# Kernel tuning notes

Hardware: AMD Instinct MI355X
Metric: run time of the kernel (lower is better)

The kernel has to match this reference:

```python
import jax, jax.numpy as jnp
import numpy as np

N_NODES = 20000
N_EDGES = 200000
MUL = 16          # multiplicity of 0e and 1o in irreps_in/out
NUM_BASIS = 8
HIDDEN = 64
W_NUMEL = 4 * MUL * MUL  # 1024: four 'uvw' paths of 16x1x16 weights
INV_SQRT3 = 1.0 / np.sqrt(3.0)
PW0 = np.sqrt(1.0 / 32.0)  # path weight into 0e: sqrt(dim(0e)/(16+16))
PW1 = np.sqrt(3.0 / 32.0)  # path weight into 1o: sqrt(dim(1o)/(16+16))
SI_NORM = 1.0 / np.sqrt(MUL)  # o3.Linear fan-in normalization


def setup_inputs() -> dict:
    key = jax.random.key(0)
    ks = jax.random.split(key, 12)
    node_feat = jax.random.normal(ks[0], (N_NODES, 4 * MUL), dtype=jnp.float32)
    edge_attr = jax.random.uniform(ks[1], (N_EDGES, NUM_BASIS), dtype=jnp.float32)
    sh = jax.random.normal(ks[2], (N_EDGES, 4), dtype=jnp.float32)
    edge_index = jax.random.randint(ks[3], (2, N_EDGES), 0, N_NODES, dtype=jnp.int32)
    # radial MLP params (torch nn.Linear: y = x @ W.T + b; we store W already transposed)
    w1 = jax.random.normal(ks[4], (NUM_BASIS, HIDDEN), dtype=jnp.float32) * 0.3
    b1 = jax.random.normal(ks[5], (HIDDEN,), dtype=jnp.float32) * 0.1
    w2 = jax.random.normal(ks[6], (HIDDEN, W_NUMEL), dtype=jnp.float32) * 0.1
    b2 = jax.random.normal(ks[7], (W_NUMEL,), dtype=jnp.float32) * 0.1
    # o3.Linear self-interaction: one (mul_in, mul_out) block per irrep
    wsi0 = jax.random.normal(ks[8], (MUL, MUL), dtype=jnp.float32)
    wsi1 = jax.random.normal(ks[9], (MUL, MUL), dtype=jnp.float32)
    return {"node_feat": node_feat, "edge_attr": edge_attr, "sh": sh,
            "w1": w1, "b1": b1, "w2": w2, "b2": b2,
            "wsi0": wsi0, "wsi1": wsi1, "edge_index": edge_index}


def reference(node_feat, edge_attr, sh, w1, b1, w2, b2, wsi0, wsi1, edge_index):
    n_nodes = node_feat.shape[0]
    row, col = edge_index[0], edge_index[1]

    # per-edge tensor-product weights from radial basis
    h = jax.nn.silu(edge_attr @ w1 + b1)
    w = h @ w2 + b2                                   # [E, 1024]
    Wp = w.reshape(-1, 4, MUL, MUL)                    # 4 paths, each (u, w)

    # gathered source-node features, split into 0e scalars and 1o vectors
    xs = node_feat[col, :MUL]                          # [E, 16]
    xv = node_feat[col, MUL:].reshape(-1, MUL, 3)      # [E, 16, 3]
    y0 = sh[:, 0]                                      # [E]   0e part of sh
    y1 = sh[:, 1:4]                                    # [E,3] 1o part of sh

    # CG paths (e3nn FullyConnectedTensorProduct, component/element norm):
    # path0: 0e x 0e -> 0e (cg=1); path3: 1o x 1o -> 0e (cg=delta/sqrt3)
    dot = jnp.einsum('eum,em->eu', xv, y1)             # [E,16]
    out0 = PW0 * (jnp.einsum('euw,eu->ew', Wp[:, 0], xs * y0[:, None])
                  + INV_SQRT3 * jnp.einsum('euw,eu->ew', Wp[:, 3], dot))
    # path1: 0e x 1o -> 1o; path2: 1o x 0e -> 1o (cg=delta/sqrt3)
    outv = (PW1 * INV_SQRT3) * (
        jnp.einsum('euw,eu->ew', Wp[:, 1], xs)[:, :, None] * y1[:, None, :]
        + jnp.einsum('euw,eum->ewm', Wp[:, 2], xv) * y0[:, None, None])

    messages = jnp.concatenate([out0, outv.reshape(-1, 3 * MUL)], axis=-1)  # [E,64]
    agg = jax.ops.segment_sum(messages, row, num_segments=n_nodes)          # [N,64]

    # self-interaction: o3.Linear (block-diagonal per irrep, / sqrt(fan_in))
    si0 = (node_feat[:, :MUL] @ wsi0) * SI_NORM
    siv = jnp.einsum('num,uw->nwm', node_feat[:, MUL:].reshape(-1, MUL, 3), wsi1) * SI_NORM
    si = jnp.concatenate([si0, siv.reshape(-1, 3 * MUL)], axis=-1)
    return agg + si
```

## Files before the change

### kernel.cpp

```cpp
#include <hip/hip_runtime.h>
#include <hip/hip_bf16.h>

#define N_NODES_C 20000
#define N_EDGES_C 200000

#define PW0_C       0.17677669529663687f
#define PW1_C       0.30618621784789724f
#define INV_SQRT3_C 0.57735026918962576f
#define SI_NORM_C   0.25f

typedef __attribute__((ext_vector_type(8))) short short8;
typedef __attribute__((ext_vector_type(4))) float f32x4;

__device__ __forceinline__ unsigned short f2bf(float x) {
    union { float f; unsigned u; } v; v.f = x;
    unsigned r = v.u + 0x7fffu + ((v.u >> 16) & 1u);
    return (unsigned short)(r >> 16);
}

__global__ __launch_bounds__(256) void k_h(const float* __restrict__ ea,
                                           const float* __restrict__ w1,
                                           const float* __restrict__ b1,
                                           unsigned short* __restrict__ h) {
    int idx = blockIdx.x * 256 + threadIdx.x;
    int e = idx >> 6, c = idx & 63;
    const float* a = ea + e * 8;
    float acc = b1[c];
    #pragma unroll
    for (int k = 0; k < 8; ++k) acc = fmaf(a[k], w1[k * 64 + c], acc);
    float s = acc / (1.0f + __expf(-acc));
    h[idx] = f2bf(s);
}

__global__ __launch_bounds__(256) void k_w2(const float* __restrict__ w2,
                                            unsigned short* __restrict__ w2f) {
    int tid = blockIdx.x * 256 + threadIdx.x;
    int j  = tid & 7;
    int l  = (tid >> 3) & 63;
    int ks = (tid >> 9) & 1;
    int tp = tid >> 10;
    int u = tp >> 2, k = tp & 3;
    int krow = ks * 32 + (l >> 4) * 8 + j;
    int col  = k * 256 + u * 16 + (l & 15);
    w2f[tid] = f2bf(w2[krow * 1024 + col]);
}

__global__ __launch_bounds__(256) void k_count(const int* __restrict__ ei,
                                               int* __restrict__ cnt) {
    int e = blockIdx.x * 256 + threadIdx.x;
    if (e < N_EDGES_C) atomicAdd(&cnt[ei[e]], 1);
}

__global__ __launch_bounds__(1024) void k_scan(const int* __restrict__ cnt,
                                               int* __restrict__ base) {
    __shared__ int wsum[16];
    __shared__ int carry_s;
    if (threadIdx.x == 0) carry_s = 0;
    int lane = threadIdx.x & 63, wid = threadIdx.x >> 6;
    __syncthreads();
    for (int start = 0; start < N_NODES_C; start += 1024) {
        int i = start + threadIdx.x;
        int v = (i < N_NODES_C) ? cnt[i] : 0;
        int x = v;
        #pragma unroll
        for (int d = 1; d < 64; d <<= 1) {
            int y = __shfl_up(x, d);
            if (lane >= d) x += y;
        }
        if (lane == 63) wsum[wid] = x;
        __syncthreads();
        int woff = 0;
        #pragma unroll
        for (int w = 0; w < 16; ++w) if (w < wid) woff += wsum[w];
        int carry = carry_s;
        if (i < N_NODES_C) base[i] = carry + woff + x - v;
        __syncthreads();
        if (threadIdx.x == 1023) carry_s = carry + woff + x;
    }
    if (threadIdx.x == 0) base[N_NODES_C] = N_EDGES_C;
}

__global__ __launch_bounds__(256) void k_fill(const int* __restrict__ ei,
                                              const int* __restrict__ base,
                                              int* __restrict__ cur,
                                              int* __restrict__ eix) {
    int e = blockIdx.x * 256 + threadIdx.x;
    if (e < N_EDGES_C) {
        int r = ei[e];
        int p = atomicAdd(&cur[r], 1);
        eix[base[r] + p] = e;
    }
}

__global__ __launch_bounds__(256, 2) void k_main(const float* __restrict__ nf,
                                                 const float* __restrict__ sh,
                                                 const int* __restrict__ ei,
                                                 const unsigned short* __restrict__ h,
                                                 const unsigned short* __restrict__ w2f,
                                                 const float* __restrict__ b2,
                                                 float* __restrict__ msg) {
    __shared__ __align__(16) char uni[24576];
    __shared__ float S[6][16][64];
    __shared__ float sh_s[64][4];
    __shared__ float b2_s[4][16][16];

    float (*nf_s)[64] = (float (*)[64])uni;
    float (*P0)[16]   = (float (*)[16])uni;
    float (*P1)[16]   = (float (*)[16])(uni + 4096);
    float (*P3)[16]   = (float (*)[16])(uni + 8192);
    float (*Q)[64][16] = (float (*)[64][16])(uni + 12288);

    const int t    = threadIdx.x;
    const int e0   = blockIdx.x * 64;
    const int lane = t & 63;
    const int wid  = t >> 6;

    {
        float* b2flat = &b2_s[0][0][0];
        #pragma unroll
        for (int i = 0; i < 4; ++i) b2flat[t + i * 256] = b2[t + i * 256];
        int el = t >> 2, part = t & 3;
        int col = ei[N_EDGES_C + e0 + el];
        const f32x4* src = (const f32x4*)(nf + col * 64);
        #pragma unroll
        for (int q = 0; q < 4; ++q)
            *(f32x4*)&nf_s[el][part * 16 + q * 4] = src[part * 4 + q];
        if (part == 0)
            *(f32x4*)&sh_s[el][0] = *(const f32x4*)(sh + (e0 + el) * 4);
    }
    short8 B0[16], B1[16];
    {
        const unsigned short* wk = w2f + wid * 1024 + lane * 8;
        #pragma unroll
        for (int u = 0; u < 16; ++u) {
            B0[u] = *(const short8*)&wk[u * 4096];
            B1[u] = *(const short8*)&wk[u * 4096 + 512];
        }
    }
    __syncthreads();

    {
        int el = t >> 2, part = t & 3;
        float y0 = sh_s[el][0], y1x = sh_s[el][1], y1y = sh_s[el][2], y1z = sh_s[el][3];
        #pragma unroll
        for (int uu = 0; uu < 4; ++uu) {
            int u = part * 4 + uu;
            float xs = nf_s[el][u];
            float v0 = nf_s[el][16 + u * 3 + 0];
            float v1 = nf_s[el][16 + u * 3 + 1];
            float v2 = nf_s[el][16 + u * 3 + 2];
            float dot = v0 * y1x + v1 * y1y + v2 * y1z;
            S[0][u][el] = xs * y0;
            S[1][u][el] = xs;
            S[2][u][el] = v0;
            S[3][u][el] = v1;
            S[4][u][el] = v2;
            S[5][u][el] = INV_SQRT3_C * dot;
        }
    }
    __syncthreads();

    const int wcol = lane & 15;
    const int g4   = (lane >> 4) << 2;

    #define TILE_PROLOG(tt)                                                          \
        const unsigned short* hrow = h + (size_t)(e0 + (tt) * 16 + (lane & 15)) * 64 \
                                       + ((lane >> 4) * 8);                          \
        short8 a0 = *(const short8*)(hrow);                                          \
        short8 a1 = *(const short8*)(hrow + 32);

    if (wid == 0) {
        #pragma unroll 1
        for (int tt = 0; tt < 4; ++tt) {
            TILE_PROLOG(tt)
            f32x4 acc = {0.f, 0.f, 0.f, 0.f};
            #pragma unroll
            for (int u = 0; u < 16; ++u) {
                f32x4 c = {0.f, 0.f, 0.f, 0.f};
                c = __builtin_amdgcn_mfma_f32_16x16x32_bf16(a0, B0[u], c, 0, 0, 0);
                c = __builtin_amdgcn_mfma_f32_16x16x32_bf16(a1, B1[u], c, 0, 0, 0);
                float bb = b2_s[0][u][wcol];
                f32x4 s = *(const f32x4*)&S[0][u][tt * 16 + g4];
                #pragma unroll
                for (int r = 0; r < 4; ++r) acc[r] = fmaf(c[r] + bb, s[r], acc[r]);
            }
            #pragma unroll
            for (int r = 0; r < 4; ++r) P0[tt * 16 + g4 + r][wcol] = acc[r];
        }
    } else if (wid == 1) {
        #pragma unroll 1
        for (int tt = 0; tt < 4; ++tt) {
            TILE_PROLOG(tt)
            f32x4 acc = {0.f, 0.f, 0.f, 0.f};
            #pragma unroll
            for (int u = 0; u < 16; ++u) {
                f32x4 c = {0.f, 0.f, 0.f, 0.f};
                c = __builtin_amdgcn_mfma_f32_16x16x32_bf16(a0, B0[u], c, 0, 0, 0);
                c = __builtin_amdgcn_mfma_f32_16x16x32_bf16(a1, B1[u], c, 0, 0, 0);
                float bb = b2_s[1][u][wcol];
                f32x4 s = *(const f32x4*)&S[1][u][tt * 16 + g4];
                #pragma unroll
                for (int r = 0; r < 4; ++r) acc[r] = fmaf(c[r] + bb, s[r], acc[r]);
            }
            #pragma unroll
            for (int r = 0; r < 4; ++r) P1[tt * 16 + g4 + r][wcol] = acc[r];
        }
    } else if (wid == 2) {
        #pragma unroll 1
        for (int tt = 0; tt < 4; ++tt) {
            TILE_PROLOG(tt)
            f32x4 qa = {0.f,0.f,0.f,0.f}, qb = {0.f,0.f,0.f,0.f}, qc = {0.f,0.f,0.f,0.f};
            #pragma unroll
            for (int u = 0; u < 16; ++u) {
                f32x4 c = {0.f, 0.f, 0.f, 0.f};
                c = __builtin_amdgcn_mfma_f32_16x16x32_bf16(a0, B0[u], c, 0, 0, 0);
                c = __builtin_amdgcn_mfma_f32_16x16x32_bf16(a1, B1[u], c, 0, 0, 0);
                float bb = b2_s[2][u][wcol];
                f32x4 s0 = *(const f32x4*)&S[2][u][tt * 16 + g4];
                f32x4 s1 = *(const f32x4*)&S[3][u][tt * 16 + g4];
                f32x4 s2 = *(const f32x4*)&S[4][u][tt * 16 + g4];
                #pragma unroll
                for (int r = 0; r < 4; ++r) {
                    float wp = c[r] + bb;
                    qa[r] = fmaf(wp, s0[r], qa[r]);
                    qb[r] = fmaf(wp, s1[r], qb[r]);
                    qc[r] = fmaf(wp, s2[r], qc[r]);
                }
            }
            #pragma unroll
            for (int r = 0; r < 4; ++r) {
                Q[0][tt * 16 + g4 + r][wcol] = qa[r];
                Q[1][tt * 16 + g4 + r][wcol] = qb[r];
                Q[2][tt * 16 + g4 + r][wcol] = qc[r];
            }
        }
    } else {
        #pragma unroll 1
        for (int tt = 0; tt < 4; ++tt) {
            TILE_PROLOG(tt)
            f32x4 acc = {0.f, 0.f, 0.f, 0.f};
            #pragma unroll
            for (int u = 0; u < 16; ++u) {
                f32x4 c = {0.f, 0.f, 0.f, 0.f};
                c = __builtin_amdgcn_mfma_f32_16x16x32_bf16(a0, B0[u], c, 0, 0, 0);
                c = __builtin_amdgcn_mfma_f32_16x16x32_bf16(a1, B1[u], c, 0, 0, 0);
                float bb = b2_s[3][u][wcol];
                f32x4 s = *(const f32x4*)&S[5][u][tt * 16 + g4];
                #pragma unroll
                for (int r = 0; r < 4; ++r) acc[r] = fmaf(c[r] + bb, s[r], acc[r]);
            }
            #pragma unroll
            for (int r = 0; r < 4; ++r) P3[tt * 16 + g4 + r][wcol] = acc[r];
        }
    }
    #undef TILE_PROLOG
    __syncthreads();

    {
        int c  = t & 63;
        int eg = t >> 6;
        if (c < 16) {
            #pragma unroll
            for (int i = 0; i < 16; ++i) {
                int e = eg * 16 + i;
                msg[(size_t)(e0 + e) * 64 + c] = PW0_C * (P0[e][c] + P3[e][c]);
            }
        } else {
            const float c1 = PW1_C * INV_SQRT3_C;
            int w = (c - 16) / 3, m = (c - 16) - 3 * w;
            #pragma unroll
            for (int i = 0; i < 16; ++i) {
                int e = eg * 16 + i;
                msg[(size_t)(e0 + e) * 64 + c] =
                    c1 * (P1[e][w] * sh_s[e][1 + m] + Q[m][e][w] * sh_s[e][0]);
            }
        }
    }
}

__global__ __launch_bounds__(256) void k_gather(const float* __restrict__ msg,
                                                const int* __restrict__ eix,
                                                const int* __restrict__ base,
                                                const float* __restrict__ nf,
                                                const float* __restrict__ wsi0,
                                                const float* __restrict__ wsi1,
                                                float* __restrict__ out) {
    int wid = threadIdx.x >> 6, lane = threadIdx.x & 63;
    int n = blockIdx.x * 4 + wid;
    if (n >= N_NODES_C) return;
    int b0 = base[n], b1 = base[n + 1];
    float acc = 0.f;
    int j = b0;
    for (; j + 4 <= b1; j += 4) {
        int ea0 = eix[j], ea1 = eix[j + 1], ea2 = eix[j + 2], ea3 = eix[j + 3];
        float v0 = msg[(size_t)ea0 * 64 + lane];
        float v1 = msg[(size_t)ea1 * 64 + lane];
        float v2 = msg[(size_t)ea2 * 64 + lane];
        float v3 = msg[(size_t)ea3 * 64 + lane];
        acc += (v0 + v1) + (v2 + v3);
    }
    for (; j < b1; ++j) acc += msg[(size_t)eix[j] * 64 + lane];
    const float* x = nf + n * 64;
    float si = 0.f;
    if (lane < 16) {
        #pragma unroll
        for (int u = 0; u < 16; ++u) si = fmaf(x[u], wsi0[u * 16 + lane], si);
    } else {
        int w = (lane - 16) / 3, m = (lane - 16) - w * 3;
        #pragma unroll
        for (int u = 0; u < 16; ++u) si = fmaf(x[16 + u * 3 + m], wsi1[u * 16 + w], si);
    }
    out[n * 64 + lane] = acc + si * SI_NORM_C;
}

extern "C" void kernel_launch(void* const* d_in, const int* in_sizes, int n_in,
                              void* d_out, int out_size, void* d_ws, size_t ws_size,
                              hipStream_t stream) {
    const float* nf   = (const float*)d_in[0];
    const float* ea   = (const float*)d_in[1];
    const float* sh   = (const float*)d_in[2];
    const float* w1   = (const float*)d_in[3];
    const float* b1   = (const float*)d_in[4];
    const float* w2   = (const float*)d_in[5];
    const float* b2   = (const float*)d_in[6];
    const float* wsi0 = (const float*)d_in[7];
    const float* wsi1 = (const float*)d_in[8];
    const int*   ei   = (const int*)d_in[9];
    float* out = (float*)d_out;

    char* ws = (char*)d_ws;
    float* msg           = (float*)ws;
    unsigned short* h    = (unsigned short*)(ws + 51200000);
    unsigned short* w2f  = (unsigned short*)(ws + 51200000 + 25600000);
    int* cnt             = (int*)(ws + 51200000 + 25600000 + 131072);
    int* cur             = cnt + N_NODES_C;
    int* base            = cur + N_NODES_C;
    int* eix             = base + N_NODES_C + 1;

    hipMemsetAsync(cnt, 0, 2 * N_NODES_C * sizeof(int), stream);

    k_h    <<<50000, 256, 0, stream>>>(ea, w1, b1, h);
    k_w2   <<<256,   256, 0, stream>>>(w2, w2f);
    k_count<<<(N_EDGES_C + 255) / 256, 256, 0, stream>>>(ei, cnt);
    k_scan <<<1,    1024, 0, stream>>>(cnt, base);
    k_fill <<<(N_EDGES_C + 255) / 256, 256, 0, stream>>>(ei, base, cur, eix);
    k_main <<<3125,  256, 0, stream>>>(nf, sh, ei, h, w2f, b2, msg);
    k_gather<<<5000, 256, 0, stream>>>(msg, eix, base, nf, wsi0, wsi1, out);
}
```

Before: 202.4 us.

## Process edges in destination-sorted order and store messages as bf16

The main kernel now visits edges in CSR (destination-sorted) order through eix, gathering h rows, sh and source features indirectly, and writes each message at its sorted position. The gather kernel can then read a contiguous run of messages per node instead of indirect scattered rows. Messages are stored as bf16, which halves write and read traffic but lowers accumulation precision. The cost is indirect reads of h and sh in the main kernel.

```diff
diff --git a/kernel.cpp b/kernel.cpp
--- a/kernel.cpp
+++ b/kernel.cpp
@@ -16,6 +16,9 @@
     union { float f; unsigned u; } v; v.f = x;
     unsigned r = v.u + 0x7fffu + ((v.u >> 16) & 1u);
     return (unsigned short)(r >> 16);
+}
+__device__ __forceinline__ float bf2f(unsigned short v) {
+    union { unsigned u; float f; } x; x.u = ((unsigned)v) << 16; return x.f;
 }
 
 __global__ __launch_bounds__(256) void k_h(const float* __restrict__ ea,
@@ -92,23 +95,25 @@
     }
 }
 
-__global__ __launch_bounds__(256, 2) void k_main(const float* __restrict__ nf,
-                                                 const float* __restrict__ sh,
-                                                 const int* __restrict__ ei,
-                                                 const unsigned short* __restrict__ h,
-                                                 const unsigned short* __restrict__ w2f,
-                                                 const float* __restrict__ b2,
-                                                 float* __restrict__ msg) {
-    __shared__ __align__(16) char uni[24576];
+__global__ void __launch_bounds__(256) __attribute__((amdgpu_waves_per_eu(2, 2)))
+k_main(const float* __restrict__ nf,
+       const float* __restrict__ sh,
+       const int* __restrict__ ei,
+       const int* __restrict__ eix,
+       const unsigned short* __restrict__ h,
+       const unsigned short* __restrict__ w2f,
+       const float* __restrict__ b2,
+       unsigned short* __restrict__ msgb) {
+    __shared__ __align__(16) char EXraw[24576];
     __shared__ float S[6][16][64];
     __shared__ float sh_s[64][4];
     __shared__ float b2_s[4][16][16];
 
-    float (*nf_s)[64] = (float (*)[64])uni;
-    float (*P0)[16]   = (float (*)[16])uni;
-    float (*P1)[16]   = (float (*)[16])(uni + 4096);
-    float (*P3)[16]   = (float (*)[16])(uni + 8192);
-    float (*Q)[64][16] = (float (*)[64][16])(uni + 12288);
+    float (*nf_s)[64]  = (float (*)[64])EXraw;
+    float (*P0)[16]    = (float (*)[16])EXraw;
+    float (*P1)[16]    = (float (*)[16])(EXraw + 4096);
+    float (*P3)[16]    = (float (*)[16])(EXraw + 8192);
+    float (*Q)[64][16] = (float (*)[64][16])(EXraw + 12288);
 
     const int t    = threadIdx.x;
     const int e0   = blockIdx.x * 64;
@@ -120,13 +125,14 @@
         #pragma unroll
         for (int i = 0; i < 4; ++i) b2flat[t + i * 256] = b2[t + i * 256];
         int el = t >> 2, part = t & 3;
-        int col = ei[N_EDGES_C + e0 + el];
-        const f32x4* src = (const f32x4*)(nf + col * 64);
+        int ep  = eix[e0 + el];
+        int col = ei[N_EDGES_C + ep];
+        const f32x4* src = (const f32x4*)(nf + (size_t)col * 64);
         #pragma unroll
         for (int q = 0; q < 4; ++q)
             *(f32x4*)&nf_s[el][part * 16 + q * 4] = src[part * 4 + q];
         if (part == 0)
-            *(f32x4*)&sh_s[el][0] = *(const f32x4*)(sh + (e0 + el) * 4);
+            *(f32x4*)&sh_s[el][0] = *(const f32x4*)(sh + (size_t)ep * 4);
     }
     short8 B0[16], B1[16];
     {
@@ -163,10 +169,10 @@
     const int wcol = lane & 15;
     const int g4   = (lane >> 4) << 2;
 
-    #define TILE_PROLOG(tt)                                                          \
-        const unsigned short* hrow = h + (size_t)(e0 + (tt) * 16 + (lane & 15)) * 64 \
-                                       + ((lane >> 4) * 8);                          \
-        short8 a0 = *(const short8*)(hrow);                                          \
+    #define TILE_PROLOG(tt)                                                        \
+        int epl = eix[e0 + (tt) * 16 + (lane & 15)];                               \
+        const unsigned short* hrow = h + (size_t)epl * 64 + ((lane >> 4) * 8);     \
+        short8 a0 = *(const short8*)(hrow);                                        \
         short8 a1 = *(const short8*)(hrow + 32);
 
     if (wid == 0) {
@@ -263,7 +269,7 @@
             #pragma unroll
             for (int i = 0; i < 16; ++i) {
                 int e = eg * 16 + i;
-                msg[(size_t)(e0 + e) * 64 + c] = PW0_C * (P0[e][c] + P3[e][c]);
+                msgb[(size_t)(e0 + e) * 64 + c] = f2bf(PW0_C * (P0[e][c] + P3[e][c]));
             }
         } else {
             const float c1 = PW1_C * INV_SQRT3_C;
@@ -271,15 +277,14 @@
             #pragma unroll
             for (int i = 0; i < 16; ++i) {
                 int e = eg * 16 + i;
-                msg[(size_t)(e0 + e) * 64 + c] =
-                    c1 * (P1[e][w] * sh_s[e][1 + m] + Q[m][e][w] * sh_s[e][0]);
-            }
-        }
-    }
-}
-
-__global__ __launch_bounds__(256) void k_gather(const float* __restrict__ msg,
-                                                const int* __restrict__ eix,
+                msgb[(size_t)(e0 + e) * 64 + c] =
+                    f2bf(c1 * (P1[e][w] * sh_s[e][1 + m] + Q[m][e][w] * sh_s[e][0]));
+            }
+        }
+    }
+}
+
+__global__ __launch_bounds__(256) void k_gather(const unsigned short* __restrict__ msgb,
                                                 const int* __restrict__ base,
                                                 const float* __restrict__ nf,
                                                 const float* __restrict__ wsi0,
@@ -288,19 +293,20 @@
     int wid = threadIdx.x >> 6, lane = threadIdx.x & 63;
     int n = blockIdx.x * 4 + wid;
     if (n >= N_NODES_C) return;
-    int b0 = base[n], b1 = base[n + 1];
+    int j0 = base[n], j1 = base[n + 1];
+    int d = j1 - j0;
+    const unsigned short* p = msgb + (size_t)j0 * 64 + lane;
     float acc = 0.f;
-    int j = b0;
-    for (; j + 4 <= b1; j += 4) {
-        int ea0 = eix[j], ea1 = eix[j + 1], ea2 = eix[j + 2], ea3 = eix[j + 3];
-        float v0 = msg[(size_t)ea0 * 64 + lane];
-        float v1 = msg[(size_t)ea1 * 64 + lane];
-        float v2 = msg[(size_t)ea2 * 64 + lane];
-        float v3 = msg[(size_t)ea3 * 64 + lane];
-        acc += (v0 + v1) + (v2 + v3);
-    }
-    for (; j < b1; ++j) acc += msg[(size_t)eix[j] * 64 + lane];
-    const float* x = nf + n * 64;
+    int j = 0;
+    for (; j + 4 <= d; j += 4) {
+        unsigned short v0 = p[(size_t)(j + 0) * 64];
+        unsigned short v1 = p[(size_t)(j + 1) * 64];
+        unsigned short v2 = p[(size_t)(j + 2) * 64];
+        unsigned short v3 = p[(size_t)(j + 3) * 64];
+        acc += (bf2f(v0) + bf2f(v1)) + (bf2f(v2) + bf2f(v3));
+    }
+    for (; j < d; ++j) acc += bf2f(p[(size_t)j * 64]);
+    const float* x = nf + (size_t)n * 64;
     float si = 0.f;
     if (lane < 16) {
         #pragma unroll
@@ -310,7 +316,7 @@
         #pragma unroll
         for (int u = 0; u < 16; ++u) si = fmaf(x[16 + u * 3 + m], wsi1[u * 16 + w], si);
     }
-    out[n * 64 + lane] = acc + si * SI_NORM_C;
+    out[(size_t)n * 64 + lane] = acc + si * SI_NORM_C;
 }
 
 extern "C" void kernel_launch(void* const* d_in, const int* in_sizes, int n_in,
@@ -329,10 +335,10 @@
     float* out = (float*)d_out;
 
     char* ws = (char*)d_ws;
-    float* msg           = (float*)ws;
-    unsigned short* h    = (unsigned short*)(ws + 51200000);
-    unsigned short* w2f  = (unsigned short*)(ws + 51200000 + 25600000);
-    int* cnt             = (int*)(ws + 51200000 + 25600000 + 131072);
+    unsigned short* msgb = (unsigned short*)ws;
+    unsigned short* h    = (unsigned short*)(ws + 25600000);
+    unsigned short* w2f  = (unsigned short*)(ws + 51200000);
+    int* cnt             = (int*)(ws + 51331072);
     int* cur             = cnt + N_NODES_C;
     int* base            = cur + N_NODES_C;
     int* eix             = base + N_NODES_C + 1;
@@ -344,6 +350,6 @@
     k_count<<<(N_EDGES_C + 255) / 256, 256, 0, stream>>>(ei, cnt);
     k_scan <<<1,    1024, 0, stream>>>(cnt, base);
     k_fill <<<(N_EDGES_C + 255) / 256, 256, 0, stream>>>(ei, base, cur, eix);
-    k_main <<<3125,  256, 0, stream>>>(nf, sh, ei, h, w2f, b2, msg);
-    k_gather<<<5000, 256, 0, stream>>>(msg, eix, base, nf, wsi0, wsi1, out);
-}
+    k_main <<<3125,  256, 0, stream>>>(nf, sh, ei, eix, h, w2f, b2, msgb);
+    k_gather<<<5000, 256, 0, stream>>>(msgb, base, nf, wsi0, wsi1, out);
+}
```

Measured after the change: 206.5 us. 2.1% more time.
